# Performance work log

Measured on AMD Instinct MI355X. Metric: run time of the kernel, lower is better.

## Reference

```python
import jax, jax.numpy as jnp
import numpy as np

N = 8192
IN_DIM = 128
OUT_DIM = 128


def setup_inputs() -> dict:
    key = jax.random.key(0)
    k_adj, k_feat, k_w = jax.random.split(key, 3)
    raw = jax.random.uniform(k_adj, (N, N), dtype=jnp.float32)
    adj = jnp.where(raw > 0.99, jnp.float32(1.0), jnp.float32(0.0))
    features = jax.random.normal(k_feat, (N, IN_DIM), dtype=jnp.float32)
    W = jax.random.normal(k_w, (OUT_DIM, IN_DIM), dtype=jnp.float32) * (1.0 / np.sqrt(IN_DIM))
    b = jnp.zeros((OUT_DIM,), dtype=jnp.float32)
    return {"adj": adj, "features": features, "W": W, "b": b}


def reference(adj, features, W, b):
    # adj + I  (original builds a sparse identity then densifies)
    n = adj.shape[0]
    adj = adj + jnp.eye(n, dtype=adj.dtype)
    row_sum = jnp.sum(adj, axis=1)                      # [N]
    d_inv_sqrt = jnp.power(row_sum, -0.5)
    d_inv_sqrt = jnp.where(jnp.isinf(d_inv_sqrt), 0.0, d_inv_sqrt)
    # diag(d) @ adj @ diag(d) == broadcast scale rows and cols (same math)
    norm_adj = d_inv_sqrt[:, None] * adj * d_inv_sqrt[None, :]
    out = norm_adj @ features                           # [N, in_dim]
    out = out @ W.T + b                                 # linear
    return jax.nn.relu(out)
```

## Files before the change

### kernel.cpp

```cpp
#include <hip/hip_runtime.h>
#include <hip/hip_bf16.h>

#define NROWS 8192
#define DIM 128
#define CAP 192

__global__ __launch_bounds__(256) void k1_scan(const float* __restrict__ adj,
                                               unsigned* __restrict__ counts,
                                               unsigned short* __restrict__ idx) {
    int row = blockIdx.x;
    __shared__ unsigned s_cnt;
    if (threadIdx.x == 0) s_cnt = 0;
    __syncthreads();
    const float4* arow = (const float4*)(adj + (size_t)row * NROWS);
    unsigned short* irow = idx + (size_t)row * CAP;
#pragma unroll
    for (int k = 0; k < 8; ++k) {
        int v4 = k * 256 + threadIdx.x;
        float4 v = arow[v4];
        int base = v4 * 4;
        if (v.x != 0.f) { unsigned p = atomicAdd(&s_cnt, 1u); if (p < CAP) irow[p] = (unsigned short)(base + 0); }
        if (v.y != 0.f) { unsigned p = atomicAdd(&s_cnt, 1u); if (p < CAP) irow[p] = (unsigned short)(base + 1); }
        if (v.z != 0.f) { unsigned p = atomicAdd(&s_cnt, 1u); if (p < CAP) irow[p] = (unsigned short)(base + 2); }
        if (v.w != 0.f) { unsigned p = atomicAdd(&s_cnt, 1u); if (p < CAP) irow[p] = (unsigned short)(base + 3); }
    }
    __syncthreads();
    if (threadIdx.x == 0) counts[row] = s_cnt;
}

#define K2ROWS 16
__global__ __launch_bounds__(256) void k2_gemm(const float* __restrict__ feat,
                                               const float* __restrict__ W,
                                               const unsigned* __restrict__ counts,
                                               float* __restrict__ d,
                                               __hip_bfloat16* __restrict__ h) {
    __shared__ __align__(16) float sWt[128][132];
    __shared__ __align__(16) float sF[K2ROWS][128];
    __shared__ float s_d[K2ROWS];
    int t = threadIdx.x;
    int row0 = blockIdx.x * K2ROWS;

#pragma unroll
    for (int it = 0; it < 16; ++it) {
        int f4 = it * 256 + t;
        float4 wv = ((const float4*)W)[f4];
        int c = f4 >> 5;
        int k = (f4 & 31) * 4;
        sWt[k + 0][c] = wv.x; sWt[k + 1][c] = wv.y;
        sWt[k + 2][c] = wv.z; sWt[k + 3][c] = wv.w;
    }
#pragma unroll
    for (int it = 0; it < 2; ++it) {
        int idx4 = it * 256 + t;
        float4 fv = ((const float4*)(feat + (size_t)row0 * DIM))[idx4];
        int r = idx4 >> 5;
        int k = (idx4 & 31) * 4;
        sF[r][k + 0] = fv.x; sF[r][k + 1] = fv.y;
        sF[r][k + 2] = fv.z; sF[r][k + 3] = fv.w;
    }
    if (t < K2ROWS) {
        float dv = rsqrtf((float)(counts[row0 + t] + 1u));
        s_d[t] = dv;
        d[row0 + t] = dv;
    }
    __syncthreads();

    int r2 = (t >> 5) * 2;
    int c4 = (t & 31) * 4;
    float acc[2][4] = {{0.f,0.f,0.f,0.f},{0.f,0.f,0.f,0.f}};
#pragma unroll 4
    for (int k = 0; k < 128; ++k) {
        float4 wv = *(const float4*)&sWt[k][c4];
        float f0 = sF[r2][k];
        float f1 = sF[r2 + 1][k];
        acc[0][0] = fmaf(f0, wv.x, acc[0][0]);
        acc[0][1] = fmaf(f0, wv.y, acc[0][1]);
        acc[0][2] = fmaf(f0, wv.z, acc[0][2]);
        acc[0][3] = fmaf(f0, wv.w, acc[0][3]);
        acc[1][0] = fmaf(f1, wv.x, acc[1][0]);
        acc[1][1] = fmaf(f1, wv.y, acc[1][1]);
        acc[1][2] = fmaf(f1, wv.z, acc[1][2]);
        acc[1][3] = fmaf(f1, wv.w, acc[1][3]);
    }
#pragma unroll
    for (int rr = 0; rr < 2; ++rr) {
        float dv = s_d[r2 + rr];
        size_t o = (size_t)(row0 + r2 + rr) * DIM + c4;
#pragma unroll
        for (int cc = 0; cc < 4; ++cc)
            h[o + cc] = __float2bfloat16(acc[rr][cc] * dv);
    }
}

__device__ __forceinline__ float bflo(unsigned p) { return __uint_as_float(p << 16); }
__device__ __forceinline__ float bfhi(unsigned p) { return __uint_as_float(p & 0xffff0000u); }

__global__ __launch_bounds__(256) void k3_gather(const unsigned* __restrict__ counts,
                                                 const unsigned short* __restrict__ idx,
                                                 const unsigned* __restrict__ h32,
                                                 const float* __restrict__ d,
                                                 const float* __restrict__ b,
                                                 float* __restrict__ out) {
    __shared__ unsigned short s_idx[4][CAP];
    int w = threadIdx.x >> 6, l = threadIdx.x & 63;
    int row = (blockIdx.x << 2) + w;
    unsigned cnt = counts[row];
    if (cnt > CAP) cnt = CAP;
    const unsigned short* irow = idx + (size_t)row * CAP;
    for (unsigned e = l; e < cnt; e += 64) s_idx[w][e] = irow[e];
    __syncthreads();

    float a0, a1;
    { unsigned p = h32[(size_t)row * 64 + l]; a0 = bflo(p); a1 = bfhi(p); }
    unsigned e = 0;
    for (; e + 4 <= cnt; e += 4) {
        int j0 = s_idx[w][e + 0];
        int j1 = s_idx[w][e + 1];
        int j2 = s_idx[w][e + 2];
        int j3 = s_idx[w][e + 3];
        unsigned p0 = h32[(size_t)j0 * 64 + l];
        unsigned p1 = h32[(size_t)j1 * 64 + l];
        unsigned p2 = h32[(size_t)j2 * 64 + l];
        unsigned p3 = h32[(size_t)j3 * 64 + l];
        a0 += bflo(p0); a1 += bfhi(p0);
        a0 += bflo(p1); a1 += bfhi(p1);
        a0 += bflo(p2); a1 += bfhi(p2);
        a0 += bflo(p3); a1 += bfhi(p3);
    }
    for (; e < cnt; ++e) {
        unsigned p = h32[(size_t)s_idx[w][e] * 64 + l];
        a0 += bflo(p); a1 += bfhi(p);
    }
    float dv = d[row];
    float2 bb = ((const float2*)b)[l];
    float o0 = fmaxf(fmaf(dv, a0, bb.x), 0.f);
    float o1 = fmaxf(fmaf(dv, a1, bb.y), 0.f);
    ((float2*)out)[(size_t)row * 64 + l] = make_float2(o0, o1);
}

extern "C" void kernel_launch(void* const* d_in, const int* in_sizes, int n_in,
                              void* d_out, int out_size, void* d_ws, size_t ws_size,
                              hipStream_t stream) {
    const float* adj  = (const float*)d_in[0];
    const float* feat = (const float*)d_in[1];
    const float* W    = (const float*)d_in[2];
    const float* b    = (const float*)d_in[3];
    float* out = (float*)d_out;

    char* ws = (char*)d_ws;
    unsigned*       counts = (unsigned*)ws;
    float*          d      = (float*)(ws + 32768);
    __hip_bfloat16* h      = (__hip_bfloat16*)(ws + 65536);
    unsigned short* idx    = (unsigned short*)(ws + 65536 + 2097152);

    k1_scan<<<NROWS, 256, 0, stream>>>(adj, counts, idx);
    k2_gemm<<<NROWS / K2ROWS, 256, 0, stream>>>(feat, W, counts, d, h);
    k3_gather<<<NROWS / 4, 256, 0, stream>>>(counts, idx, (const unsigned*)h, d, b, out);
}
```

Measured before the change: 71.95 us.

## Encode adjacency as wave-ballot bitmasks and expand to indices in gather

The scan kernel no longer uses per-nonzero shared atomics to build index lists. Each wave ballots nonzero flags and writes 64-bit masks, then counts are reduced from popcounts. The gather kernel reads the 1 KB per-row bitmask, expands it into column indices in shared memory with one atomic per lane, and decodes the interleaved bit layout. This removes the serialized atomics from the bandwidth-bound scan, at the cost of extra decode work and a changed summation order in the gather.

```diff
diff --git a/kernel.cpp b/kernel.cpp
--- a/kernel.cpp
+++ b/kernel.cpp
@@ -4,28 +4,33 @@
 #define NROWS 8192
 #define DIM 128
 #define CAP 192
+#define WPR 128
 
 __global__ __launch_bounds__(256) void k1_scan(const float* __restrict__ adj,
                                                unsigned* __restrict__ counts,
-                                               unsigned short* __restrict__ idx) {
+                                               unsigned long long* __restrict__ bm) {
     int row = blockIdx.x;
-    __shared__ unsigned s_cnt;
-    if (threadIdx.x == 0) s_cnt = 0;
-    __syncthreads();
+    int t = threadIdx.x, lane = t & 63, w = t >> 6;
     const float4* arow = (const float4*)(adj + (size_t)row * NROWS);
-    unsigned short* irow = idx + (size_t)row * CAP;
+    unsigned long long* brow = bm + (size_t)row * WPR;
+    __shared__ unsigned s_c[4];
+    unsigned my = 0;
 #pragma unroll
     for (int k = 0; k < 8; ++k) {
-        int v4 = k * 256 + threadIdx.x;
-        float4 v = arow[v4];
-        int base = v4 * 4;
-        if (v.x != 0.f) { unsigned p = atomicAdd(&s_cnt, 1u); if (p < CAP) irow[p] = (unsigned short)(base + 0); }
-        if (v.y != 0.f) { unsigned p = atomicAdd(&s_cnt, 1u); if (p < CAP) irow[p] = (unsigned short)(base + 1); }
-        if (v.z != 0.f) { unsigned p = atomicAdd(&s_cnt, 1u); if (p < CAP) irow[p] = (unsigned short)(base + 2); }
-        if (v.w != 0.f) { unsigned p = atomicAdd(&s_cnt, 1u); if (p < CAP) irow[p] = (unsigned short)(base + 3); }
+        float4 v = arow[k * 256 + t];
+        unsigned long long m0 = __ballot(v.x != 0.f);
+        unsigned long long m1 = __ballot(v.y != 0.f);
+        unsigned long long m2 = __ballot(v.z != 0.f);
+        unsigned long long m3 = __ballot(v.w != 0.f);
+        if (lane == 0) {
+            unsigned long long* p = brow + (size_t)(k * 4 + w) * 4;
+            p[0] = m0; p[1] = m1; p[2] = m2; p[3] = m3;
+            my += (unsigned)(__popcll(m0) + __popcll(m1) + __popcll(m2) + __popcll(m3));
+        }
     }
+    if (lane == 0) s_c[w] = my;
     __syncthreads();
-    if (threadIdx.x == 0) counts[row] = s_cnt;
+    if (t == 0) counts[row] = s_c[0] + s_c[1] + s_c[2] + s_c[3];
 }
 
 #define K2ROWS 16
@@ -95,20 +100,38 @@
 __device__ __forceinline__ float bflo(unsigned p) { return __uint_as_float(p << 16); }
 __device__ __forceinline__ float bfhi(unsigned p) { return __uint_as_float(p & 0xffff0000u); }
 
-__global__ __launch_bounds__(256) void k3_gather(const unsigned* __restrict__ counts,
-                                                 const unsigned short* __restrict__ idx,
+__global__ __launch_bounds__(256) void k3_gather(const unsigned long long* __restrict__ bm,
                                                  const unsigned* __restrict__ h32,
                                                  const float* __restrict__ d,
                                                  const float* __restrict__ b,
                                                  float* __restrict__ out) {
     __shared__ unsigned short s_idx[4][CAP];
+    __shared__ unsigned s_cnt[4];
     int w = threadIdx.x >> 6, l = threadIdx.x & 63;
     int row = (blockIdx.x << 2) + w;
-    unsigned cnt = counts[row];
+    if (l == 0) s_cnt[w] = 0;
+    __syncthreads();
+
+    const unsigned long long* brow = bm + (size_t)row * WPR;
+    unsigned long long wd0 = brow[l];
+    unsigned long long wd1 = brow[l + 64];
+    unsigned pc = (unsigned)(__popcll(wd0) + __popcll(wd1));
+    unsigned off = pc ? atomicAdd(&s_cnt[w], pc) : 0u;
+    {
+        unsigned long long m = wd0; int W = l;
+        while (m && off < CAP) {
+            int i = __ffsll((long long)m) - 1; m &= m - 1;
+            s_idx[w][off++] = (unsigned short)(((W >> 2) << 8) | (i << 2) | (W & 3));
+        }
+        m = wd1; W = l + 64;
+        while (m && off < CAP) {
+            int i = __ffsll((long long)m) - 1; m &= m - 1;
+            s_idx[w][off++] = (unsigned short)(((W >> 2) << 8) | (i << 2) | (W & 3));
+        }
+    }
+    __syncthreads();
+    unsigned cnt = s_cnt[w];
     if (cnt > CAP) cnt = CAP;
-    const unsigned short* irow = idx + (size_t)row * CAP;
-    for (unsigned e = l; e < cnt; e += 64) s_idx[w][e] = irow[e];
-    __syncthreads();
 
     float a0, a1;
     { unsigned p = h32[(size_t)row * 64 + l]; a0 = bflo(p); a1 = bfhi(p); }
@@ -148,12 +171,12 @@
     float* out = (float*)d_out;
 
     char* ws = (char*)d_ws;
-    unsigned*       counts = (unsigned*)ws;
-    float*          d      = (float*)(ws + 32768);
-    __hip_bfloat16* h      = (__hip_bfloat16*)(ws + 65536);
-    unsigned short* idx    = (unsigned short*)(ws + 65536 + 2097152);
+    unsigned*           counts = (unsigned*)ws;
+    float*              d      = (float*)(ws + 32768);
+    __hip_bfloat16*     h      = (__hip_bfloat16*)(ws + 65536);
+    unsigned long long* bmask  = (unsigned long long*)(ws + 65536 + 2097152);
 
-    k1_scan<<<NROWS, 256, 0, stream>>>(adj, counts, idx);
+    k1_scan<<<NROWS, 256, 0, stream>>>(adj, counts, bmask);
     k2_gemm<<<NROWS / K2ROWS, 256, 0, stream>>>(feat, W, counts, d, h);
-    k3_gather<<<NROWS / 4, 256, 0, stream>>>(counts, idx, (const unsigned*)h, d, b, out);
+    k3_gather<<<NROWS / 4, 256, 0, stream>>>(bmask, (const unsigned*)h, d, b, out);
 }
```

Result: slower. 73.82 us (+2.6%).

## Fuse adjacency scan and feature GEMM into one launch, move column scaling into gather

Applied to the files above, without the earlier changes.

Merges the adjacency scan kernel and the feature×W GEMM into a single launch where the first blocks compute the GEMM and the remaining blocks scan adjacency rows. Because the GEMM no longer waits for degree counts, the column-side d_j scaling moves into the gather kernel, which loads d[j] per neighbour. W is now stored in shared memory as bf16 with an XOR swizzle, and each block handles 8 rows. The intent is to remove a launch boundary and let the compute-bound GEMM overlap the bandwidth-bound 256 MB adjacency read. The cost is extra d[j] loads in the gather and reduced W precision.

```diff
diff --git a/kernel.cpp b/kernel.cpp
--- a/kernel.cpp
+++ b/kernel.cpp
@@ -4,91 +4,84 @@
 #define NROWS 8192
 #define DIM 128
 #define CAP 192
+#define GEMMBLKS 1024
 
-__global__ __launch_bounds__(256) void k1_scan(const float* __restrict__ adj,
-                                               unsigned* __restrict__ counts,
-                                               unsigned short* __restrict__ idx) {
-    int row = blockIdx.x;
-    __shared__ unsigned s_cnt;
-    if (threadIdx.x == 0) s_cnt = 0;
-    __syncthreads();
-    const float4* arow = (const float4*)(adj + (size_t)row * NROWS);
-    unsigned short* irow = idx + (size_t)row * CAP;
-#pragma unroll
-    for (int k = 0; k < 8; ++k) {
-        int v4 = k * 256 + threadIdx.x;
-        float4 v = arow[v4];
-        int base = v4 * 4;
-        if (v.x != 0.f) { unsigned p = atomicAdd(&s_cnt, 1u); if (p < CAP) irow[p] = (unsigned short)(base + 0); }
-        if (v.y != 0.f) { unsigned p = atomicAdd(&s_cnt, 1u); if (p < CAP) irow[p] = (unsigned short)(base + 1); }
-        if (v.z != 0.f) { unsigned p = atomicAdd(&s_cnt, 1u); if (p < CAP) irow[p] = (unsigned short)(base + 2); }
-        if (v.w != 0.f) { unsigned p = atomicAdd(&s_cnt, 1u); if (p < CAP) irow[p] = (unsigned short)(base + 3); }
-    }
-    __syncthreads();
-    if (threadIdx.x == 0) counts[row] = s_cnt;
+__device__ __forceinline__ unsigned short f2bf(float f) {
+    unsigned u = __float_as_uint(f);
+    u += 0x7fffu + ((u >> 16) & 1u);
+    return (unsigned short)(u >> 16);
 }
 
-#define K2ROWS 16
-__global__ __launch_bounds__(256) void k2_gemm(const float* __restrict__ feat,
-                                               const float* __restrict__ W,
-                                               const unsigned* __restrict__ counts,
-                                               float* __restrict__ d,
-                                               __hip_bfloat16* __restrict__ h) {
-    __shared__ __align__(16) float sWt[128][132];
-    __shared__ __align__(16) float sF[K2ROWS][128];
-    __shared__ float s_d[K2ROWS];
-    int t = threadIdx.x;
-    int row0 = blockIdx.x * K2ROWS;
+__global__ __launch_bounds__(256) void k12(const float* __restrict__ adj,
+                                           const float* __restrict__ feat,
+                                           const float* __restrict__ Wm,
+                                           unsigned* __restrict__ counts,
+                                           float* __restrict__ d,
+                                           unsigned short* __restrict__ idx,
+                                           __hip_bfloat16* __restrict__ h) {
+    __shared__ unsigned short sW[16384];
+    __shared__ __align__(16) float sX[8][128];
+    __shared__ unsigned s_cnt;
+    const int t = threadIdx.x;
 
+    if (blockIdx.x < GEMMBLKS) {
+        const int row0 = blockIdx.x << 3;
 #pragma unroll
-    for (int it = 0; it < 16; ++it) {
-        int f4 = it * 256 + t;
-        float4 wv = ((const float4*)W)[f4];
-        int c = f4 >> 5;
-        int k = (f4 & 31) * 4;
-        sWt[k + 0][c] = wv.x; sWt[k + 1][c] = wv.y;
-        sWt[k + 2][c] = wv.z; sWt[k + 3][c] = wv.w;
-    }
+        for (int it = 0; it < 16; ++it) {
+            int i4 = it * 256 + t;
+            float4 wv = ((const float4*)Wm)[i4];
+            int wc = i4 >> 5, kc = i4 & 31;
+            unsigned short* p = &sW[(wc << 7) + ((kc ^ (wc & 31)) << 2)];
+            p[0] = f2bf(wv.x); p[1] = f2bf(wv.y); p[2] = f2bf(wv.z); p[3] = f2bf(wv.w);
+        }
+        {
+            float4 fv = ((const float4*)(feat + (size_t)row0 * DIM))[t];
+            *(float4*)&sX[t >> 5][(t & 31) << 2] = fv;
+        }
+        __syncthreads();
+
+        const int c = t & 127, r0 = (t >> 7) << 2, cswz = c & 31;
+        float acc[4] = {0.f, 0.f, 0.f, 0.f};
 #pragma unroll
-    for (int it = 0; it < 2; ++it) {
-        int idx4 = it * 256 + t;
-        float4 fv = ((const float4*)(feat + (size_t)row0 * DIM))[idx4];
-        int r = idx4 >> 5;
-        int k = (idx4 & 31) * 4;
-        sF[r][k + 0] = fv.x; sF[r][k + 1] = fv.y;
-        sF[r][k + 2] = fv.z; sF[r][k + 3] = fv.w;
-    }
-    if (t < K2ROWS) {
-        float dv = rsqrtf((float)(counts[row0 + t] + 1u));
-        s_d[t] = dv;
-        d[row0 + t] = dv;
-    }
-    __syncthreads();
-
-    int r2 = (t >> 5) * 2;
-    int c4 = (t & 31) * 4;
-    float acc[2][4] = {{0.f,0.f,0.f,0.f},{0.f,0.f,0.f,0.f}};
-#pragma unroll 4
-    for (int k = 0; k < 128; ++k) {
-        float4 wv = *(const float4*)&sWt[k][c4];
-        float f0 = sF[r2][k];
-        float f1 = sF[r2 + 1][k];
-        acc[0][0] = fmaf(f0, wv.x, acc[0][0]);
-        acc[0][1] = fmaf(f0, wv.y, acc[0][1]);
-        acc[0][2] = fmaf(f0, wv.z, acc[0][2]);
-        acc[0][3] = fmaf(f0, wv.w, acc[0][3]);
-        acc[1][0] = fmaf(f1, wv.x, acc[1][0]);
-        acc[1][1] = fmaf(f1, wv.y, acc[1][1]);
-        acc[1][2] = fmaf(f1, wv.z, acc[1][2]);
-        acc[1][3] = fmaf(f1, wv.w, acc[1][3]);
-    }
+        for (int KK = 0; KK < 32; ++KK) {
+            unsigned long long wv8 = *(const unsigned long long*)&sW[(c << 7) + ((KK ^ cswz) << 2)];
+            unsigned wlo = (unsigned)wv8, whi = (unsigned)(wv8 >> 32);
+            float w0 = __uint_as_float(wlo << 16), w1 = __uint_as_float(wlo & 0xffff0000u);
+            float w2 = __uint_as_float(whi << 16), w3 = __uint_as_float(whi & 0xffff0000u);
+            const int kb = KK << 2;
+            float4 x0 = *(const float4*)&sX[r0 + 0][kb];
+            float4 x1 = *(const float4*)&sX[r0 + 1][kb];
+            float4 x2 = *(const float4*)&sX[r0 + 2][kb];
+            float4 x3 = *(const float4*)&sX[r0 + 3][kb];
+            acc[0] = fmaf(x0.x, w0, fmaf(x0.y, w1, fmaf(x0.z, w2, fmaf(x0.w, w3, acc[0]))));
+            acc[1] = fmaf(x1.x, w0, fmaf(x1.y, w1, fmaf(x1.z, w2, fmaf(x1.w, w3, acc[1]))));
+            acc[2] = fmaf(x2.x, w0, fmaf(x2.y, w1, fmaf(x2.z, w2, fmaf(x2.w, w3, acc[2]))));
+            acc[3] = fmaf(x3.x, w0, fmaf(x3.y, w1, fmaf(x3.z, w2, fmaf(x3.w, w3, acc[3]))));
+        }
 #pragma unroll
-    for (int rr = 0; rr < 2; ++rr) {
-        float dv = s_d[r2 + rr];
-        size_t o = (size_t)(row0 + r2 + rr) * DIM + c4;
+        for (int i = 0; i < 4; ++i)
+            h[(size_t)(row0 + r0 + i) * DIM + c] = __float2bfloat16(acc[i]);
+    } else {
+        const int row = blockIdx.x - GEMMBLKS;
+        if (t == 0) s_cnt = 0;
+        __syncthreads();
+        const float4* arow = (const float4*)(adj + (size_t)row * NROWS);
+        unsigned short* irow = idx + (size_t)row * CAP;
 #pragma unroll
-        for (int cc = 0; cc < 4; ++cc)
-            h[o + cc] = __float2bfloat16(acc[rr][cc] * dv);
+        for (int k = 0; k < 8; ++k) {
+            int v4 = k * 256 + t;
+            float4 v = arow[v4];
+            int base = v4 * 4;
+            if (v.x != 0.f) { unsigned p = atomicAdd(&s_cnt, 1u); if (p < CAP) irow[p] = (unsigned short)(base + 0); }
+            if (v.y != 0.f) { unsigned p = atomicAdd(&s_cnt, 1u); if (p < CAP) irow[p] = (unsigned short)(base + 1); }
+            if (v.z != 0.f) { unsigned p = atomicAdd(&s_cnt, 1u); if (p < CAP) irow[p] = (unsigned short)(base + 2); }
+            if (v.w != 0.f) { unsigned p = atomicAdd(&s_cnt, 1u); if (p < CAP) irow[p] = (unsigned short)(base + 3); }
+        }
+        __syncthreads();
+        if (t == 0) {
+            counts[row] = s_cnt;
+            d[row] = rsqrtf((float)(s_cnt + 1u));
+        }
     }
 }
 
@@ -110,28 +103,31 @@
     for (unsigned e = l; e < cnt; e += 64) s_idx[w][e] = irow[e];
     __syncthreads();
 
+    float dv = d[row];
     float a0, a1;
-    { unsigned p = h32[(size_t)row * 64 + l]; a0 = bflo(p); a1 = bfhi(p); }
+    { unsigned p = h32[(size_t)row * 64 + l]; a0 = dv * bflo(p); a1 = dv * bfhi(p); }
     unsigned e = 0;
     for (; e + 4 <= cnt; e += 4) {
         int j0 = s_idx[w][e + 0];
         int j1 = s_idx[w][e + 1];
         int j2 = s_idx[w][e + 2];
         int j3 = s_idx[w][e + 3];
+        float dj0 = d[j0], dj1 = d[j1], dj2 = d[j2], dj3 = d[j3];
         unsigned p0 = h32[(size_t)j0 * 64 + l];
         unsigned p1 = h32[(size_t)j1 * 64 + l];
         unsigned p2 = h32[(size_t)j2 * 64 + l];
         unsigned p3 = h32[(size_t)j3 * 64 + l];
-        a0 += bflo(p0); a1 += bfhi(p0);
-        a0 += bflo(p1); a1 += bfhi(p1);
-        a0 += bflo(p2); a1 += bfhi(p2);
-        a0 += bflo(p3); a1 += bfhi(p3);
+        a0 = fmaf(dj0, bflo(p0), a0); a1 = fmaf(dj0, bfhi(p0), a1);
+        a0 = fmaf(dj1, bflo(p1), a0); a1 = fmaf(dj1, bfhi(p1), a1);
+        a0 = fmaf(dj2, bflo(p2), a0); a1 = fmaf(dj2, bfhi(p2), a1);
+        a0 = fmaf(dj3, bflo(p3), a0); a1 = fmaf(dj3, bfhi(p3), a1);
     }
     for (; e < cnt; ++e) {
-        unsigned p = h32[(size_t)s_idx[w][e] * 64 + l];
-        a0 += bflo(p); a1 += bfhi(p);
+        int j = s_idx[w][e];
+        float dj = d[j];
+        unsigned p = h32[(size_t)j * 64 + l];
+        a0 = fmaf(dj, bflo(p), a0); a1 = fmaf(dj, bfhi(p), a1);
     }
-    float dv = d[row];
     float2 bb = ((const float2*)b)[l];
     float o0 = fmaxf(fmaf(dv, a0, bb.x), 0.f);
     float o1 = fmaxf(fmaf(dv, a1, bb.y), 0.f);
@@ -153,7 +149,6 @@
     __hip_bfloat16* h      = (__hip_bfloat16*)(ws + 65536);
     unsigned short* idx    = (unsigned short*)(ws + 65536 + 2097152);
 
-    k1_scan<<<NROWS, 256, 0, stream>>>(adj, counts, idx);
-    k2_gemm<<<NROWS / K2ROWS, 256, 0, stream>>>(feat, W, counts, d, h);
+    k12<<<GEMMBLKS + NROWS, 256, 0, stream>>>(adj, feat, W, counts, d, idx, h);
     k3_gather<<<NROWS / 4, 256, 0, stream>>>(counts, idx, (const unsigned*)h, d, b, out);
 }
```

Measured after the change: 83.31 us. +15.8%, slower.
